# Optimization experiments

Hardware: AMD Instinct MI355X
Metric: run time of the kernel (lower is better)

Reference implementation:

```python
import jax, jax.numpy as jnp
import numpy as np

NUM_STEPS = 50
STEP_SIZE = 0.1
SPARSE_MULT = 0.3


def setup_inputs() -> dict:
    key = jax.random.key(0)
    k1, k2 = jax.random.split(key)
    input_tensor = jax.random.normal(k1, (16384, 784), dtype=jnp.float32)
    w = jax.random.normal(k2, (784, 1024), dtype=jnp.float32)
    # L2-normalize dictionary columns (dim=0), as in __init__
    w = w / jnp.linalg.norm(w, axis=0, keepdims=True)
    return {"input_tensor": input_tensor, "w": w}


def _threshold(u):
    # soft threshold with rectification: a = relu(u - lambda)
    return jnp.where(u > SPARSE_MULT, u - SPARSE_MULT, jnp.zeros_like(u))


def reference(input_tensor, w):
    num_latent = w.shape[1]
    b = input_tensor @ w                                  # [B, L] excitatory drive
    g = w.T @ w - jnp.eye(num_latent, dtype=w.dtype)      # [L, L] lateral inhibition

    u0 = jnp.zeros((input_tensor.shape[0], num_latent), dtype=input_tensor.dtype)

    def step(u, _):
        a = _threshold(u)
        du = b - a @ g - u
        return u + STEP_SIZE * du, None

    u_final, _ = jax.lax.scan(step, u0, None, length=NUM_STEPS - 1)
    a_final = _threshold(u_final)
    reconstruction = a_final @ w.T                        # [B, 784]
    return reconstruction
```

## Files before the change

kernel.cpp:

```cpp
#include <hip/hip_runtime.h>

#define NROWS 16384
#define DIN   784
#define DPAD  800
#define NLAT  1024
#define BM    64
#define ASTRIDE 1032
#define NITER 48

typedef __attribute__((ext_vector_type(8))) short  short8;
typedef __attribute__((ext_vector_type(4))) float  f32x4;

__device__ __forceinline__ unsigned short f2bf(float f) {
    unsigned int u = __builtin_bit_cast(unsigned int, f);
    u += 0x7fffu + ((u >> 16) & 1u);
    return (unsigned short)(u >> 16);
}


__global__ void convert_w_kernel(const float* __restrict__ w, unsigned short* __restrict__ wbf) {
    int i = blockIdx.x * 256 + threadIdx.x;
    wbf[i] = f2bf(w[i]);
}

__global__ void transpose_pad_kernel(const float* __restrict__ w, unsigned short* __restrict__ wT) {
    __shared__ float tile[32][33];
    int d0 = blockIdx.x * 32;
    int l0 = blockIdx.y * 32;
    int tx = threadIdx.x, ty = threadIdx.y;
    int d = d0 + ty;
    tile[ty][tx] = (d < DIN) ? w[(size_t)d * NLAT + l0 + tx] : 0.f;
    __syncthreads();
    wT[(size_t)(l0 + ty) * DPAD + d0 + tx] = f2bf(tile[tx][ty]);
}

__global__ void gram_kernel(const float* __restrict__ w, unsigned short* __restrict__ g) {
    __shared__ float Wk[32][33];
    __shared__ float Wl[32][33];
    int k0 = blockIdx.x * 32, l0 = blockIdx.y * 32;
    int t = threadIdx.x;
    int c = t & 31, r8 = t >> 5;
    float acc[4] = {0.f, 0.f, 0.f, 0.f};
    for (int d0 = 0; d0 < DPAD; d0 += 32) {
        __syncthreads();
        #pragma unroll
        for (int rr = 0; rr < 4; ++rr) {
            int d = d0 + r8 + rr * 8;
            float vk = 0.f, vl = 0.f;
            if (d < DIN) {
                vk = w[(size_t)d * NLAT + k0 + c];
                vl = w[(size_t)d * NLAT + l0 + c];
            }
            Wk[r8 + rr * 8][c] = vk;
            Wl[r8 + rr * 8][c] = vl;
        }
        __syncthreads();
        #pragma unroll
        for (int dd = 0; dd < 32; ++dd) {
            float bl = Wl[dd][c];
            #pragma unroll
            for (int rr = 0; rr < 4; ++rr)
                acc[rr] += Wk[dd][r8 + rr * 8] * bl;
        }
    }
    #pragma unroll
    for (int rr = 0; rr < 4; ++rr) {
        int kr = k0 + r8 + rr * 8;
        int lc = l0 + c;
        float v = acc[rr] - ((kr == lc) ? 1.f : 0.f);
        g[(size_t)kr * NLAT + lc] = f2bf(v);
    }
}


__global__ __launch_bounds__(512, 2) void lca_main_kernel(
    const float* __restrict__ x,
    const unsigned short* __restrict__ g,
    const unsigned short* __restrict__ wbf,
    const unsigned short* __restrict__ wT,
    float* __restrict__ out)
{
    extern __shared__ char smem[];
    unsigned short* a_lds = (unsigned short*)smem;
    unsigned short* x_lds = (unsigned short*)(smem + BM * ASTRIDE * 2);

    const int tid  = threadIdx.x;
    const int lane = tid & 63;
    const int wv   = tid >> 6;
    const int l15  = lane & 15;
    const int lg   = lane >> 4;
    const int rowbase = blockIdx.x * BM;
    const int wcol = wv * 128;

    f32x4 acc[4][8];
    #pragma unroll
    for (int mt = 0; mt < 4; ++mt)
        #pragma unroll
        for (int nt = 0; nt < 8; ++nt)
            acc[mt][nt] = (f32x4){0.f, 0.f, 0.f, 0.f};

    const int srow = tid >> 3;
    const int sq   = tid & 7;
    {
        int k = sq * 4;
        float4 v = make_float4(0.f, 0.f, 0.f, 0.f);
        if (k < DIN) v = *(const float4*)(x + (size_t)(rowbase + srow) * DIN + k);
        unsigned short* dst = x_lds + srow * 40 + sq * 4;
        *(unsigned int*)(dst)     = (unsigned int)f2bf(v.x) | ((unsigned int)f2bf(v.y) << 16);
        *(unsigned int*)(dst + 2) = (unsigned int)f2bf(v.z) | ((unsigned int)f2bf(v.w) << 16);
    }
    __syncthreads();
    for (int kc = 0; kc < 25; ++kc) {
        if (kc < 24) {
            int k = (kc + 1) * 32 + sq * 4;
            float4 v = make_float4(0.f, 0.f, 0.f, 0.f);
            if (k < DIN) v = *(const float4*)(x + (size_t)(rowbase + srow) * DIN + k);
            unsigned short* dst = x_lds + ((kc + 1) & 1) * (BM * 40) + srow * 40 + sq * 4;
            *(unsigned int*)(dst)     = (unsigned int)f2bf(v.x) | ((unsigned int)f2bf(v.y) << 16);
            *(unsigned int*)(dst + 2) = (unsigned int)f2bf(v.z) | ((unsigned int)f2bf(v.w) << 16);
        }
        const int buf = kc & 1;
        short8 af[4];
        #pragma unroll
        for (int mt = 0; mt < 4; ++mt)
            af[mt] = *(const short8*)(x_lds + buf * (BM * 40) + (mt * 16 + l15) * 40 + lg * 8);
        #pragma unroll
        for (int nt = 0; nt < 8; ++nt) {
            short8 bfr = *(const short8*)(wT + (size_t)(wcol + nt * 16 + l15) * DPAD + kc * 32 + lg * 8);
            #pragma unroll
            for (int mt = 0; mt < 4; ++mt)
                acc[mt][nt] = __builtin_amdgcn_mfma_f32_16x16x32_bf16(af[mt], bfr, acc[mt][nt], 0, 0, 0);
        }
        __syncthreads();
    }

    unsigned int bpk[4][8][2];
    #pragma unroll
    for (int mt = 0; mt < 4; ++mt)
        #pragma unroll
        for (int nt = 0; nt < 8; ++nt) {
            bpk[mt][nt][0] = (unsigned int)f2bf(acc[mt][nt][0]) | ((unsigned int)f2bf(acc[mt][nt][1]) << 16);
            bpk[mt][nt][1] = (unsigned int)f2bf(acc[mt][nt][2]) | ((unsigned int)f2bf(acc[mt][nt][3]) << 16);
            acc[mt][nt] = -acc[mt][nt];
        }

    const unsigned short* gl = g + (size_t)(wcol + l15) * NLAT + lg * 8;
    const int aoff_r = l15 * ASTRIDE + lg * 8;

    for (int it = 0; it < NITER; ++it) {
        __syncthreads();
        #pragma unroll
        for (int mt = 0; mt < 4; ++mt)
            #pragma unroll
            for (int nt = 0; nt < 8; ++nt) {
                int colbase = wcol + nt * 16 + l15;
                #pragma unroll
                for (int r = 0; r < 4; ++r) {
                    int row = mt * 16 + lg * 4 + r;
                    float a = fmaxf(fmaf(-0.1f, acc[mt][nt][r], -0.3f), 0.f);
                    a_lds[row * ASTRIDE + colbase] = f2bf(a);
                }
            }
        __syncthreads();
        #pragma unroll
        for (int mt = 0; mt < 4; ++mt)
            #pragma unroll
            for (int nt = 0; nt < 8; ++nt) {
                float b0 = __builtin_bit_cast(float, bpk[mt][nt][0] << 16);
                float b1 = __builtin_bit_cast(float, bpk[mt][nt][0] & 0xffff0000u);
                float b2 = __builtin_bit_cast(float, bpk[mt][nt][1] << 16);
                float b3 = __builtin_bit_cast(float, bpk[mt][nt][1] & 0xffff0000u);
                acc[mt][nt][0] = fmaf(0.9f, acc[mt][nt][0], -b0);
                acc[mt][nt][1] = fmaf(0.9f, acc[mt][nt][1], -b1);
                acc[mt][nt][2] = fmaf(0.9f, acc[mt][nt][2], -b2);
                acc[mt][nt][3] = fmaf(0.9f, acc[mt][nt][3], -b3);
            }
        for (int kc = 0; kc < 32; ++kc) {
            short8 af[4];
            #pragma unroll
            for (int mt = 0; mt < 4; ++mt)
                af[mt] = *(const short8*)(a_lds + mt * 16 * ASTRIDE + aoff_r + kc * 32);
            #pragma unroll
            for (int ng = 0; ng < 2; ++ng) {
                short8 bfr[4];
                #pragma unroll
                for (int j = 0; j < 4; ++j)
                    bfr[j] = *(const short8*)(gl + (size_t)(ng * 4 + j) * 16 * NLAT + kc * 32);
                #pragma unroll
                for (int j = 0; j < 4; ++j)
                    #pragma unroll
                    for (int mt = 0; mt < 4; ++mt)
                        acc[mt][ng * 4 + j] =
                            __builtin_amdgcn_mfma_f32_16x16x32_bf16(af[mt], bfr[j], acc[mt][ng * 4 + j], 0, 0, 0);
            }
        }
    }

    __syncthreads();
    #pragma unroll
    for (int mt = 0; mt < 4; ++mt)
        #pragma unroll
        for (int nt = 0; nt < 8; ++nt) {
            int colbase = wcol + nt * 16 + l15;
            #pragma unroll
            for (int r = 0; r < 4; ++r) {
                int row = mt * 16 + lg * 4 + r;
                float a = fmaxf(fmaf(-0.1f, acc[mt][nt][r], -0.3f), 0.f);
                a_lds[row * ASTRIDE + colbase] = f2bf(a);
            }
        }
    __syncthreads();
    for (int nt = wv; nt < 49; nt += 8) {
        f32x4 racc[4];
        #pragma unroll
        for (int mt = 0; mt < 4; ++mt) racc[mt] = (f32x4){0.f, 0.f, 0.f, 0.f};
        for (int kc = 0; kc < 32; ++kc) {
            short8 af[4];
            #pragma unroll
            for (int mt = 0; mt < 4; ++mt)
                af[mt] = *(const short8*)(a_lds + mt * 16 * ASTRIDE + aoff_r + kc * 32);
            short8 bfr = *(const short8*)(wbf + (size_t)(nt * 16 + l15) * NLAT + kc * 32 + lg * 8);
            #pragma unroll
            for (int mt = 0; mt < 4; ++mt)
                racc[mt] = __builtin_amdgcn_mfma_f32_16x16x32_bf16(af[mt], bfr, racc[mt], 0, 0, 0);
        }
        #pragma unroll
        for (int mt = 0; mt < 4; ++mt)
            #pragma unroll
            for (int r = 0; r < 4; ++r)
                out[(size_t)(rowbase + mt * 16 + lg * 4 + r) * DIN + nt * 16 + l15] = racc[mt][r];
    }
}


extern "C" void kernel_launch(void* const* d_in, const int* in_sizes, int n_in,
                              void* d_out, int out_size, void* d_ws, size_t ws_size,
                              hipStream_t stream) {
    const float* x = (const float*)d_in[0];
    const float* w = (const float*)d_in[1];
    float* out = (float*)d_out;
    char* ws = (char*)d_ws;

    unsigned short* g   = (unsigned short*)(ws);
    unsigned short* wbf = (unsigned short*)(ws + (2u << 20));
    unsigned short* wT  = (unsigned short*)(ws + (2u << 20) + DIN * NLAT * 2);

    convert_w_kernel<<<3136, 256, 0, stream>>>(w, wbf);
    transpose_pad_kernel<<<dim3(25, 32), dim3(32, 32), 0, stream>>>(w, wT);
    gram_kernel<<<dim3(32, 32), 256, 0, stream>>>(w, g);

    const int smem_bytes = BM * ASTRIDE * 2 + 2 * BM * 40 * 2;
    hipFuncSetAttribute((const void*)lca_main_kernel,
                        hipFuncAttributeMaxDynamicSharedMemorySize, smem_bytes);
    lca_main_kernel<<<256, 512, smem_bytes, stream>>>(x, g, wbf, wT, out);
}
```

Before: 4.249 ms.

## Spill b drive to output buffer, XOR-swizzle LDS, double-buffer G loads

The bf16-packed excitatory drive b is no longer held in registers. Each block writes it into its own region of the output buffer and reloads it with nontemporal loads every iteration, which cuts register pressure. The padded activation LDS stride is replaced by an XOR-swizzled 2048-byte row layout to avoid bank conflicts. The inner Gram-matrix loop is software-pipelined with double-buffered A and G fragments, and the reconstruction work is split into contiguous per-wave ranges. These changes add global memory traffic each iteration, and reusing the output buffer as scratch relies on each block overwriting only its own rows before the final stores.

Measured after the change: 11.41 ms. 168% more time.

```diff
diff --git a/kernel.cpp b/kernel.cpp
--- a/kernel.cpp
+++ b/kernel.cpp
@@ -1,21 +1,25 @@
 #include <hip/hip_runtime.h>
 
-#define NROWS 16384
 #define DIN   784
 #define DPAD  800
 #define NLAT  1024
 #define BM    64
-#define ASTRIDE 1032
 #define NITER 48
 
 typedef __attribute__((ext_vector_type(8))) short  short8;
 typedef __attribute__((ext_vector_type(4))) float  f32x4;
+typedef __attribute__((ext_vector_type(4))) unsigned int u32x4;
 
 __device__ __forceinline__ unsigned short f2bf(float f) {
     unsigned int u = __builtin_bit_cast(unsigned int, f);
     u += 0x7fffu + ((u >> 16) & 1u);
     return (unsigned short)(u >> 16);
 }
+__device__ __forceinline__ unsigned int pk2(float a, float b) {
+    return (unsigned int)f2bf(a) | ((unsigned int)f2bf(b) << 16);
+}
+__device__ __forceinline__ float bf2f_lo(unsigned int p) { return __builtin_bit_cast(float, p << 16); }
+__device__ __forceinline__ float bf2f_hi(unsigned int p) { return __builtin_bit_cast(float, p & 0xffff0000u); }
 
 
 __global__ void convert_w_kernel(const float* __restrict__ w, unsigned short* __restrict__ wbf) {
@@ -81,16 +85,20 @@
     float* __restrict__ out)
 {
     extern __shared__ char smem[];
-    unsigned short* a_lds = (unsigned short*)smem;
-    unsigned short* x_lds = (unsigned short*)(smem + BM * ASTRIDE * 2);
+    char* a_lds = smem;
+    unsigned short* x_lds = (unsigned short*)(smem + BM * 2048);
 
     const int tid  = threadIdx.x;
     const int lane = tid & 63;
     const int wv   = tid >> 6;
     const int l15  = lane & 15;
+    const int l7   = lane & 7;
     const int lg   = lane >> 4;
     const int rowbase = blockIdx.x * BM;
     const int wcol = wv * 128;
+
+    u32x4* bs4 = (u32x4*)out;
+    const size_t bsbase = (size_t)blockIdx.x * 12544 + tid;
 
     f32x4 acc[4][8];
     #pragma unroll
@@ -103,21 +111,21 @@
     const int sq   = tid & 7;
     {
         int k = sq * 4;
-        float4 v = make_float4(0.f, 0.f, 0.f, 0.f);
-        if (k < DIN) v = *(const float4*)(x + (size_t)(rowbase + srow) * DIN + k);
+        f32x4 v = (f32x4){0.f, 0.f, 0.f, 0.f};
+        if (k < DIN) v = __builtin_nontemporal_load((const f32x4*)(x + (size_t)(rowbase + srow) * DIN + k));
         unsigned short* dst = x_lds + srow * 40 + sq * 4;
-        *(unsigned int*)(dst)     = (unsigned int)f2bf(v.x) | ((unsigned int)f2bf(v.y) << 16);
-        *(unsigned int*)(dst + 2) = (unsigned int)f2bf(v.z) | ((unsigned int)f2bf(v.w) << 16);
+        *(unsigned int*)(dst)     = pk2(v.x, v.y);
+        *(unsigned int*)(dst + 2) = pk2(v.z, v.w);
     }
     __syncthreads();
     for (int kc = 0; kc < 25; ++kc) {
         if (kc < 24) {
             int k = (kc + 1) * 32 + sq * 4;
-            float4 v = make_float4(0.f, 0.f, 0.f, 0.f);
-            if (k < DIN) v = *(const float4*)(x + (size_t)(rowbase + srow) * DIN + k);
+            f32x4 v = (f32x4){0.f, 0.f, 0.f, 0.f};
+            if (k < DIN) v = __builtin_nontemporal_load((const f32x4*)(x + (size_t)(rowbase + srow) * DIN + k));
             unsigned short* dst = x_lds + ((kc + 1) & 1) * (BM * 40) + srow * 40 + sq * 4;
-            *(unsigned int*)(dst)     = (unsigned int)f2bf(v.x) | ((unsigned int)f2bf(v.y) << 16);
-            *(unsigned int*)(dst + 2) = (unsigned int)f2bf(v.z) | ((unsigned int)f2bf(v.w) << 16);
+            *(unsigned int*)(dst)     = pk2(v.x, v.y);
+            *(unsigned int*)(dst + 2) = pk2(v.z, v.w);
         }
         const int buf = kc & 1;
         short8 af[4];
@@ -134,101 +142,115 @@
         __syncthreads();
     }
 
-    unsigned int bpk[4][8][2];
+    #pragma unroll
+    for (int d4 = 0; d4 < 16; ++d4) {
+        int p0 = d4 * 2, p1 = d4 * 2 + 1;
+        u32x4 v;
+        v.x = pk2(acc[p0 >> 3][p0 & 7][0], acc[p0 >> 3][p0 & 7][1]);
+        v.y = pk2(acc[p0 >> 3][p0 & 7][2], acc[p0 >> 3][p0 & 7][3]);
+        v.z = pk2(acc[p1 >> 3][p1 & 7][0], acc[p1 >> 3][p1 & 7][1]);
+        v.w = pk2(acc[p1 >> 3][p1 & 7][2], acc[p1 >> 3][p1 & 7][3]);
+        __builtin_nontemporal_store(v, bs4 + bsbase + d4 * 512);
+    }
     #pragma unroll
     for (int mt = 0; mt < 4; ++mt)
         #pragma unroll
-        for (int nt = 0; nt < 8; ++nt) {
-            bpk[mt][nt][0] = (unsigned int)f2bf(acc[mt][nt][0]) | ((unsigned int)f2bf(acc[mt][nt][1]) << 16);
-            bpk[mt][nt][1] = (unsigned int)f2bf(acc[mt][nt][2]) | ((unsigned int)f2bf(acc[mt][nt][3]) << 16);
+        for (int nt = 0; nt < 8; ++nt)
             acc[mt][nt] = -acc[mt][nt];
-        }
-
-    const unsigned short* gl = g + (size_t)(wcol + l15) * NLAT + lg * 8;
-    const int aoff_r = l15 * ASTRIDE + lg * 8;
-
-    for (int it = 0; it < NITER; ++it) {
-        __syncthreads();
+
+    const char* gpan = (const char*)g + (size_t)__builtin_amdgcn_readfirstlane(wv * (128 * 2048));
+    const int gvoff = l15 * 2048 + lg * 16;
+
+    auto LDAF = [&](short8 (&af)[4], int kc) {
+        int colb = ((kc * 4 + lg) ^ l7) << 4;
+        #pragma unroll
+        for (int mt = 0; mt < 4; ++mt)
+            af[mt] = *(const short8*)(a_lds + (mt * 16 + l15) * 2048 + colb);
+    };
+    auto LDG = [&](short8 (&bfr)[8], int kc) {
+        #pragma unroll
+        for (int j = 0; j < 8; ++j)
+            bfr[j] = *(const short8*)(gpan + j * 32768 + gvoff + kc * 64);
+    };
+    auto MM = [&](short8 (&af)[4], short8 (&bfr)[8]) {
+        #pragma unroll
+        for (int j = 0; j < 8; ++j)
+            #pragma unroll
+            for (int mt = 0; mt < 4; ++mt)
+                acc[mt][j] = __builtin_amdgcn_mfma_f32_16x16x32_bf16(af[mt], bfr[j], acc[mt][j], 0, 0, 0);
+    };
+    auto THRW = [&]() {
         #pragma unroll
         for (int mt = 0; mt < 4; ++mt)
             #pragma unroll
             for (int nt = 0; nt < 8; ++nt) {
-                int colbase = wcol + nt * 16 + l15;
+                int chunkbase = (wcol >> 3) + nt * 2 + (l15 >> 3);
                 #pragma unroll
                 for (int r = 0; r < 4; ++r) {
                     int row = mt * 16 + lg * 4 + r;
                     float a = fmaxf(fmaf(-0.1f, acc[mt][nt][r], -0.3f), 0.f);
-                    a_lds[row * ASTRIDE + colbase] = f2bf(a);
+                    *(unsigned short*)(a_lds + row * 2048 + ((chunkbase ^ (row & 7)) << 4) + l7 * 2) = f2bf(a);
                 }
             }
+    };
+
+    short8 afA[4], afB[4], gA[8], gBf[8];
+
+    #pragma unroll 1
+    for (int it = 0; it < NITER; ++it) {
+        __syncthreads();
+        u32x4 br[16];
+        #pragma unroll
+        for (int d4 = 0; d4 < 16; ++d4)
+            br[d4] = __builtin_nontemporal_load(bs4 + bsbase + d4 * 512);
+        THRW();
         __syncthreads();
         #pragma unroll
         for (int mt = 0; mt < 4; ++mt)
             #pragma unroll
             for (int nt = 0; nt < 8; ++nt) {
-                float b0 = __builtin_bit_cast(float, bpk[mt][nt][0] << 16);
-                float b1 = __builtin_bit_cast(float, bpk[mt][nt][0] & 0xffff0000u);
-                float b2 = __builtin_bit_cast(float, bpk[mt][nt][1] << 16);
-                float b3 = __builtin_bit_cast(float, bpk[mt][nt][1] & 0xffff0000u);
-                acc[mt][nt][0] = fmaf(0.9f, acc[mt][nt][0], -b0);
-                acc[mt][nt][1] = fmaf(0.9f, acc[mt][nt][1], -b1);
-                acc[mt][nt][2] = fmaf(0.9f, acc[mt][nt][2], -b2);
-                acc[mt][nt][3] = fmaf(0.9f, acc[mt][nt][3], -b3);
+                int p = mt * 8 + nt;
+                unsigned int w0 = (p & 1) ? br[p >> 1].z : br[p >> 1].x;
+                unsigned int w1 = (p & 1) ? br[p >> 1].w : br[p >> 1].y;
+                acc[mt][nt][0] = fmaf(0.9f, acc[mt][nt][0], -bf2f_lo(w0));
+                acc[mt][nt][1] = fmaf(0.9f, acc[mt][nt][1], -bf2f_hi(w0));
+                acc[mt][nt][2] = fmaf(0.9f, acc[mt][nt][2], -bf2f_lo(w1));
+                acc[mt][nt][3] = fmaf(0.9f, acc[mt][nt][3], -bf2f_hi(w1));
             }
-        for (int kc = 0; kc < 32; ++kc) {
-            short8 af[4];
-            #pragma unroll
-            for (int mt = 0; mt < 4; ++mt)
-                af[mt] = *(const short8*)(a_lds + mt * 16 * ASTRIDE + aoff_r + kc * 32);
-            #pragma unroll
-            for (int ng = 0; ng < 2; ++ng) {
-                short8 bfr[4];
-                #pragma unroll
-                for (int j = 0; j < 4; ++j)
-                    bfr[j] = *(const short8*)(gl + (size_t)(ng * 4 + j) * 16 * NLAT + kc * 32);
-                #pragma unroll
-                for (int j = 0; j < 4; ++j)
-                    #pragma unroll
-                    for (int mt = 0; mt < 4; ++mt)
-                        acc[mt][ng * 4 + j] =
-                            __builtin_amdgcn_mfma_f32_16x16x32_bf16(af[mt], bfr[j], acc[mt][ng * 4 + j], 0, 0, 0);
-            }
-        }
-    }
-
-    __syncthreads();
-    #pragma unroll
-    for (int mt = 0; mt < 4; ++mt)
-        #pragma unroll
-        for (int nt = 0; nt < 8; ++nt) {
-            int colbase = wcol + nt * 16 + l15;
-            #pragma unroll
-            for (int r = 0; r < 4; ++r) {
-                int row = mt * 16 + lg * 4 + r;
-                float a = fmaxf(fmaf(-0.1f, acc[mt][nt][r], -0.3f), 0.f);
-                a_lds[row * ASTRIDE + colbase] = f2bf(a);
-            }
-        }
-    __syncthreads();
-    for (int nt = wv; nt < 49; nt += 8) {
+        LDAF(afA, 0); LDG(gA, 0);
+        #pragma unroll
+        for (int kc = 0; kc < 32; kc += 2) {
+            LDAF(afB, kc + 1); LDG(gBf, kc + 1);
+            MM(afA, gA);
+            if (kc + 2 < 32) { LDAF(afA, kc + 2); LDG(gA, kc + 2); }
+            MM(afB, gBf);
+        }
+    }
+
+    __syncthreads();
+    THRW();
+    __syncthreads();
+    const int nt0 = wv * 6;
+    const int ntn = (wv == 7) ? 7 : 6;
+    for (int t = 0; t < ntn; ++t) {
+        int nt = nt0 + t;
         f32x4 racc[4];
         #pragma unroll
         for (int mt = 0; mt < 4; ++mt) racc[mt] = (f32x4){0.f, 0.f, 0.f, 0.f};
         for (int kc = 0; kc < 32; ++kc) {
             short8 af[4];
+            LDAF(af, kc);
+            short8 bw = *(const short8*)(wbf + (size_t)(nt * 16 + l15) * NLAT + kc * 32 + lg * 8);
             #pragma unroll
             for (int mt = 0; mt < 4; ++mt)
-                af[mt] = *(const short8*)(a_lds + mt * 16 * ASTRIDE + aoff_r + kc * 32);
-            short8 bfr = *(const short8*)(wbf + (size_t)(nt * 16 + l15) * NLAT + kc * 32 + lg * 8);
-            #pragma unroll
-            for (int mt = 0; mt < 4; ++mt)
-                racc[mt] = __builtin_amdgcn_mfma_f32_16x16x32_bf16(af[mt], bfr, racc[mt], 0, 0, 0);
+                racc[mt] = __builtin_amdgcn_mfma_f32_16x16x32_bf16(af[mt], bw, racc[mt], 0, 0, 0);
         }
         #pragma unroll
         for (int mt = 0; mt < 4; ++mt)
             #pragma unroll
             for (int r = 0; r < 4; ++r)
-                out[(size_t)(rowbase + mt * 16 + lg * 4 + r) * DIN + nt * 16 + l15] = racc[mt][r];
+                __builtin_nontemporal_store(racc[mt][r],
+                    out + (size_t)(rowbase + mt * 16 + lg * 4 + r) * DIN + nt * 16 + l15);
     }
 }
 
@@ -249,8 +271,8 @@
     transpose_pad_kernel<<<dim3(25, 32), dim3(32, 32), 0, stream>>>(w, wT);
     gram_kernel<<<dim3(32, 32), 256, 0, stream>>>(w, g);
 
-    const int smem_bytes = BM * ASTRIDE * 2 + 2 * BM * 40 * 2;
-    hipFuncSetAttribute((const void*)lca_main_kernel,
+    const int smem_bytes = BM * 2048 + 2 * BM * 40 * 2;
+    (void)hipFuncSetAttribute((const void*)lca_main_kernel,
                         hipFuncAttributeMaxDynamicSharedMemorySize, smem_bytes);
     lca_main_kernel<<<256, 512, smem_bytes, stream>>>(x, g, wbf, wT, out);
 }
```
